# Kernel optimization log

Hardware: AMD Instinct MI355X
Metric: run time of the kernel (lower is better)

The kernel has to match this reference:

```python
import jax, jax.numpy as jnp
import numpy as np

H = 16      # num_heads
D = 1024    # input_dim
F = 4096    # feed_forward_hidden_size
B, S = 8, 4096
EPS = 1e-6


def _ln(x, g, b):
    mu = jnp.mean(x, axis=-1, keepdims=True)
    var = jnp.mean(jnp.square(x - mu), axis=-1, keepdims=True)
    return (x - mu) * jax.lax.rsqrt(var + EPS) * g + b


def _attn(Q, K, V):
    # per-head attention; original scales by sqrt(input_dim), NOT sqrt(head_dim)
    b, sq, d = Q.shape
    sk = K.shape[1]
    dh = d // H
    Qh = Q.reshape(b, sq, H, dh)
    Kh = K.reshape(b, sk, H, dh)
    Vh = V.reshape(b, sk, H, dh)
    scores = jnp.einsum('bqhd,bkhd->bhqk', Qh, Kh) / jnp.sqrt(jnp.float32(d))
    w = jax.nn.softmax(scores, axis=-1)
    return jnp.einsum('bhqk,bkhd->bqhd', w, Vh).reshape(b, sq, d)


def setup_inputs() -> dict:
    key = jax.random.key(0)
    ks = jax.random.split(key, 10)
    sc = 0.02
    np.random.seed(42)
    decode_input = jnp.asarray(np.random.random([B, 1, D]).astype(np.float32))
    return {
        'key': jax.random.normal(ks[0], (B, S, D), jnp.float32),
        'value': jax.random.normal(ks[1], (B, S, D), jnp.float32),
        'decode_input': decode_input,
        'Wq': jax.random.normal(ks[2], (D, D), jnp.float32) * sc,
        'bq': jnp.zeros((D,), jnp.float32),
        'Wk': jax.random.normal(ks[3], (D, D), jnp.float32) * sc,
        'bk': jnp.zeros((D,), jnp.float32),
        'Wv': jax.random.normal(ks[4], (D, D), jnp.float32) * sc,
        'bv': jnp.zeros((D,), jnp.float32),
        'Wo': jax.random.normal(ks[5], (D, D), jnp.float32) * sc,
        'bo': jnp.zeros((D,), jnp.float32),
        'W1': jax.random.normal(ks[6], (D, F), jnp.float32) * sc,
        'b1': jnp.zeros((F,), jnp.float32),
        'W2': jax.random.normal(ks[7], (F, D), jnp.float32) * sc,
        'b2': jnp.zeros((D,), jnp.float32),
        'ln2_g': jnp.ones((D,), jnp.float32),
        'ln2_b': jnp.zeros((D,), jnp.float32),
        'lnf_g': jnp.ones((D,), jnp.float32),
        'lnf_b': jnp.zeros((D,), jnp.float32),
    }


def reference(key, value, decode_input, Wq, bq, Wk, bk, Wv, bv, Wo, bo,
              W1, b1, W2, b2, ln2_g, ln2_b, lnf_g, lnf_b):
    # K/V projections shared by both attention calls (original reuses mha_1)
    K = key @ Wk + bk            # [B,S,D]
    V = value @ Wv + bv          # [B,S,D]

    # mha_1: self-attention of decode_input would use its own K/V, but here
    # q=k=v=decode_input for the first call
    Q1 = decode_input @ Wq + bq
    K1 = decode_input @ Wk + bk
    V1 = decode_input @ Wv + bv
    mha1_out = _attn(Q1, K1, V1) @ Wo + bo   # [B,1,D]
    # note: layer_norm_mha_1 output is computed in original but never used

    # second call (original buggily calls mha_1 again): q=mha1_out (un-normed)
    Q2 = mha1_out @ Wq + bq
    mha2_out = _attn(Q2, K, V) @ Wo + bo     # [B,1,D]
    x = _ln(mha2_out + decode_input, ln2_g, ln2_b)

    ff = jax.nn.relu(x @ W1 + b1) @ W2 + b2
    return _ln(ff + x, lnf_g, lnf_b)
```

## Files before the change

### kernel.cpp

```cpp
#include <hip/hip_runtime.h>
#include <hip/hip_bf16.h>

#define NB 8
#define NS 4096
#define ND 1024
#define NH 16
#define NF 4096

typedef __attribute__((ext_vector_type(8))) short s16x8;
typedef __attribute__((ext_vector_type(4))) float f32x4;

__device__ __forceinline__ short f2bfs(float x) {
    __hip_bfloat16 h = __float2bfloat16(x);
    return *reinterpret_cast<short*>(&h);
}

__device__ __forceinline__ s16x8 pack8(float4 a, float4 b) {
    s16x8 r;
    r[0]=f2bfs(a.x); r[1]=f2bfs(a.y); r[2]=f2bfs(a.z); r[3]=f2bfs(a.w);
    r[4]=f2bfs(b.x); r[5]=f2bfs(b.y); r[6]=f2bfs(b.z); r[7]=f2bfs(b.w);
    return r;
}


template<int KC>
__global__ void __launch_bounds__(256) mvV_k(const float* __restrict__ x,
        const float* __restrict__ W, int K, int Cout, float* __restrict__ Pout)
{
    __shared__ float xs[KC * 8];
    int tid = threadIdx.x;
    int c = blockIdx.x * 256 + tid;
    int k0 = blockIdx.y * KC;
    for (int i = tid; i < KC * 8; i += 256) {
        int k = i >> 3, b = i & 7;
        xs[i] = x[(size_t)b * K + k0 + k];
    }
    __syncthreads();
    const float* Wp = W + (size_t)k0 * Cout + c;
    float acc[8] = {0,0,0,0,0,0,0,0};
    #pragma unroll 16
    for (int k = 0; k < KC; ++k) {
        float wv = Wp[(size_t)k * Cout];
        float4 x0 = *(const float4*)&xs[k * 8];
        float4 x1 = *(const float4*)&xs[k * 8 + 4];
        acc[0] += x0.x * wv; acc[1] += x0.y * wv; acc[2] += x0.z * wv; acc[3] += x0.w * wv;
        acc[4] += x1.x * wv; acc[5] += x1.y * wv; acc[6] += x1.z * wv; acc[7] += x1.w * wv;
    }
    float* op = Pout + ((size_t)blockIdx.y * 8) * Cout + c;
    #pragma unroll
    for (int b = 0; b < 8; ++b) op[(size_t)b * Cout] = acc[b];
}

template<int KC, int NP, int RELU>
__global__ void __launch_bounds__(256) mvP_k(const float* __restrict__ P,
        const float* __restrict__ bias, const float* __restrict__ W,
        int K, int Cout, float* __restrict__ Pout)
{
    __shared__ float xs[KC * 8];
    int tid = threadIdx.x;
    int c = blockIdx.x * 256 + tid;
    int k0 = blockIdx.y * KC;
    for (int i = tid; i < KC * 8; i += 256) {
        int b = i / KC, k = i % KC;
        float t = bias[k0 + k];
        #pragma unroll 8
        for (int p = 0; p < NP; ++p) t += P[((size_t)(p * 8 + b)) * K + k0 + k];
        if (RELU) t = fmaxf(t, 0.f);
        xs[k * 8 + b] = t;
    }
    __syncthreads();
    const float* Wp = W + (size_t)k0 * Cout + c;
    float acc[8] = {0,0,0,0,0,0,0,0};
    #pragma unroll 16
    for (int k = 0; k < KC; ++k) {
        float wv = Wp[(size_t)k * Cout];
        float4 x0 = *(const float4*)&xs[k * 8];
        float4 x1 = *(const float4*)&xs[k * 8 + 4];
        acc[0] += x0.x * wv; acc[1] += x0.y * wv; acc[2] += x0.z * wv; acc[3] += x0.w * wv;
        acc[4] += x1.x * wv; acc[5] += x1.y * wv; acc[6] += x1.z * wv; acc[7] += x1.w * wv;
    }
    float* op = Pout + ((size_t)blockIdx.y * 8) * Cout + c;
    #pragma unroll
    for (int b = 0; b < 8; ++b) op[(size_t)b * Cout] = acc[b];
}

__global__ void __launch_bounds__(256) u_k(const float* __restrict__ P,
        const float* __restrict__ bq, const float* __restrict__ Wk,
        unsigned short* __restrict__ u16)
{
    int bh = blockIdx.x;
    int b = bh >> 4, h = bh & 15;
    int lane = threadIdx.x & 63, wv = threadIdx.x >> 6;
    int cc = h * 64 + lane;
    float q = bq[cc];
    #pragma unroll 8
    for (int p = 0; p < 64; ++p) q += P[((size_t)(p * 8 + b)) * 1024 + cc];
    int dbase = blockIdx.y * 256;
    #pragma unroll 4
    for (int d = dbase + wv; d < dbase + 256; d += 4) {
        float v = Wk[(size_t)d * 1024 + cc] * q;
        for (int off = 32; off; off >>= 1) v += __shfl_down(v, off);
        if (lane == 0) u16[(size_t)bh * 1024 + d] = (unsigned short)f2bfs(v);
    }
}

__global__ void __launch_bounds__(256) lnp_k(const float* __restrict__ P, int np,
        const float* __restrict__ bias, const float* __restrict__ add,
        const float* __restrict__ g, const float* __restrict__ be,
        float* __restrict__ out)
{
    int b = blockIdx.x, tid = threadIdx.x;
    __shared__ float sd[4];
    int c = tid * 4;
    f32x4 t = *(const f32x4*)&bias[c];
    t += *(const f32x4*)&add[(size_t)b * 1024 + c];
    #pragma unroll 8
    for (int p = 0; p < np; ++p)
        t += *(const f32x4*)&P[((size_t)(p * 8 + b)) * 1024 + c];
    float loc = t[0] + t[1] + t[2] + t[3];
    for (int off = 32; off; off >>= 1) loc += __shfl_down(loc, off);
    if ((tid & 63) == 0) sd[tid >> 6] = loc;
    __syncthreads();
    float mu = (sd[0] + sd[1] + sd[2] + sd[3]) * (1.f / 1024.f);
    __syncthreads();
    f32x4 d = t - mu;
    float v = d[0]*d[0] + d[1]*d[1] + d[2]*d[2] + d[3]*d[3];
    for (int off = 32; off; off >>= 1) v += __shfl_down(v, off);
    if ((tid & 63) == 0) sd[tid >> 6] = v;
    __syncthreads();
    float var = (sd[0] + sd[1] + sd[2] + sd[3]) * (1.f / 1024.f);
    float rs = rsqrtf(var + 1e-6f);
    f32x4 gg = *(const f32x4*)&g[c];
    f32x4 bb = *(const f32x4*)&be[c];
    f32x4 o = d * rs * gg + bb;
    *(f32x4*)&out[(size_t)b * 1024 + c] = o;
}

__global__ void __launch_bounds__(256) attn_k(const float* __restrict__ key,
        const float* __restrict__ value, const unsigned short* __restrict__ u16,
        float* __restrict__ plp, float* __restrict__ dnm)
{
    __shared__ __align__(16) unsigned short ul[16][1032];
    __shared__ float pl[16][64];
    int b = blockIdx.x, ch = blockIdx.y, tid = threadIdx.x;
    int s0 = ch * 64;

    const uint4* src = (const uint4*)(u16 + (size_t)b * NH * 1024);
    for (int v = tid; v < 2048; v += 256) {
        int h = v >> 7, col = (v & 127) * 8;
        *(uint4*)&ul[h][col] = src[v];
    }
    __syncthreads();

    {
        int lane = tid & 63, wv = tid >> 6;
        int r = lane & 15, g = lane >> 4;
        const float* kp0 = key + ((size_t)(b * NS + s0 + wv * 16 + r)) * ND + g * 8;
        f32x4 acc = {0.f, 0.f, 0.f, 0.f};
        float4 c0, c1, c2, c3, n0, n1, n2, n3;
        c0 = *(const float4*)(kp0);      c1 = *(const float4*)(kp0 + 4);
        c2 = *(const float4*)(kp0 + 32); c3 = *(const float4*)(kp0 + 36);
        #pragma unroll
        for (int k = 0; k < 1024; k += 64) {
            if (k + 64 < 1024) {
                const float* p = kp0 + k + 64;
                n0 = *(const float4*)(p);      n1 = *(const float4*)(p + 4);
                n2 = *(const float4*)(p + 32); n3 = *(const float4*)(p + 36);
            }
            s16x8 a0 = *(const s16x8*)&ul[r][k + g * 8];
            acc = __builtin_amdgcn_mfma_f32_16x16x32_bf16(a0, pack8(c0, c1), acc, 0, 0, 0);
            s16x8 a1 = *(const s16x8*)&ul[r][k + 32 + g * 8];
            acc = __builtin_amdgcn_mfma_f32_16x16x32_bf16(a1, pack8(c2, c3), acc, 0, 0, 0);
            c0 = n0; c1 = n1; c2 = n2; c3 = n3;
        }
        const float scl = 1.f / 32.f;
        #pragma unroll
        for (int j = 0; j < 4; ++j) {
            int h = g * 4 + j;
            pl[h][wv * 16 + r] = __expf(acc[j] * scl);
        }
    }
    __syncthreads();

    if (tid < 16) {
        float s = 0.f;
        #pragma unroll 16
        for (int si = 0; si < 64; ++si) s += pl[tid][si];
        dnm[((size_t)(ch * 8 + b)) * 16 + tid] = s;
    }

    {
        const float* vp = value + ((size_t)(b * NS + s0)) * ND + tid * 4;
        f32x4 acc[16];
        #pragma unroll
        for (int h = 0; h < 16; ++h) acc[h] = (f32x4){0.f, 0.f, 0.f, 0.f};
        f32x4 v0,v1,v2,v3,v4,v5,v6,v7;
        v0 = *(const f32x4*)(vp + 0*ND); v1 = *(const f32x4*)(vp + 1*ND);
        v2 = *(const f32x4*)(vp + 2*ND); v3 = *(const f32x4*)(vp + 3*ND);
        v4 = *(const f32x4*)(vp + 4*ND); v5 = *(const f32x4*)(vp + 5*ND);
        v6 = *(const f32x4*)(vp + 6*ND); v7 = *(const f32x4*)(vp + 7*ND);
        for (int g = 0; g < 64; g += 8) {
            f32x4 n0,n1,n2,n3,n4,n5,n6,n7;
            if (g + 8 < 64) {
                const float* p = vp + (size_t)(g + 8) * ND;
                n0 = *(const f32x4*)(p + 0*ND); n1 = *(const f32x4*)(p + 1*ND);
                n2 = *(const f32x4*)(p + 2*ND); n3 = *(const f32x4*)(p + 3*ND);
                n4 = *(const f32x4*)(p + 4*ND); n5 = *(const f32x4*)(p + 5*ND);
                n6 = *(const f32x4*)(p + 6*ND); n7 = *(const f32x4*)(p + 7*ND);
            }
            #pragma unroll
            for (int h = 0; h < 16; ++h) {
                f32x4 wa = *(const f32x4*)&pl[h][g];
                f32x4 wb = *(const f32x4*)&pl[h][g + 4];
                acc[h] += v0 * wa[0] + v1 * wa[1] + v2 * wa[2] + v3 * wa[3]
                        + v4 * wb[0] + v5 * wb[1] + v6 * wb[2] + v7 * wb[3];
            }
            v0 = n0; v1 = n1; v2 = n2; v3 = n3;
            v4 = n4; v5 = n5; v6 = n6; v7 = n7;
        }
        float* o = plp + ((size_t)((ch * 8 + b) * 16)) * 1024 + tid * 4;
        #pragma unroll
        for (int h = 0; h < 16; ++h) *(f32x4*)(o + (size_t)h * 1024) = acc[h];
    }
}

template<int KC, int NCH>
__global__ void __launch_bounds__(256) mvH_k(const float* __restrict__ plp,
        const float* __restrict__ dnm, const float* __restrict__ W,
        float* __restrict__ Pout)
{
    __shared__ float xs[4 * KC * 8];
    int tid = threadIdx.x, lane = tid & 63, wv = tid >> 6;
    int c = blockIdx.x * 256 + tid;
    int k0 = blockIdx.y * KC;
    int h = blockIdx.x * 4 + wv;
    float den = 0.f;
    if (lane < 8) {
        #pragma unroll 8
        for (int ch = 0; ch < NCH; ++ch)
            den += dnm[((size_t)(ch * 8 + lane)) * 16 + h];
    }
    float inv8 = (lane < 8) ? 1.f / den : 0.f;
    for (int i = lane; i < 8 * KC; i += 64) {
        int b = i / KC, k = i % KC;
        float t = 0.f;
        #pragma unroll 8
        for (int ch = 0; ch < NCH; ++ch)
            t += plp[((size_t)((ch * 8 + b) * 16 + h)) * 1024 + k0 + k];
        xs[wv * 8 * KC + k * 8 + b] = t * __shfl(inv8, b);
    }
    __syncthreads();
    const float* Wp = W + (size_t)k0 * 1024 + c;
    float acc[8] = {0,0,0,0,0,0,0,0};
    #pragma unroll 16
    for (int k = 0; k < KC; ++k) {
        float wvv = Wp[(size_t)k * 1024];
        float4 x0 = *(const float4*)&xs[wv * 8 * KC + k * 8];
        float4 x1 = *(const float4*)&xs[wv * 8 * KC + k * 8 + 4];
        acc[0] += x0.x * wvv; acc[1] += x0.y * wvv; acc[2] += x0.z * wvv; acc[3] += x0.w * wvv;
        acc[4] += x1.x * wvv; acc[5] += x1.y * wvv; acc[6] += x1.z * wvv; acc[7] += x1.w * wvv;
    }
    float* op = Pout + ((size_t)blockIdx.y * 8) * 1024 + c;
    #pragma unroll
    for (int b = 0; b < 8; ++b) op[(size_t)b * 1024] = acc[b];
}

extern "C" void kernel_launch(void* const* d_in, const int* in_sizes, int n_in,
                              void* d_out, int out_size, void* d_ws, size_t ws_size,
                              hipStream_t stream)
{
    const float* key   = (const float*)d_in[0];
    const float* value = (const float*)d_in[1];
    const float* dec   = (const float*)d_in[2];
    const float* Wq = (const float*)d_in[3];  const float* bq = (const float*)d_in[4];
    const float* Wk = (const float*)d_in[5];
    const float* Wv = (const float*)d_in[7];  const float* bv = (const float*)d_in[8];
    const float* Wo = (const float*)d_in[9];  const float* bo = (const float*)d_in[10];
    const float* W1 = (const float*)d_in[11]; const float* b1 = (const float*)d_in[12];
    const float* W2 = (const float*)d_in[13]; const float* b2 = (const float*)d_in[14];
    const float* g2 = (const float*)d_in[15]; const float* be2 = (const float*)d_in[16];
    const float* gf = (const float*)d_in[17]; const float* bef = (const float*)d_in[18];

    float* ws = (float*)d_ws;
    float* Pa   = ws;
    float* Pb   = Pa   + 524288;
    float* Pq   = Pb   + 524288;
    float* plp  = Pq   + 524288;
    float* dnm  = plp  + 8388608;
    float* Pd   = dnm  + 8192;
    float* Pe   = Pd   + 524288;
    float* Pff1 = Pe   + 524288;
    float* Pff2 = Pff1 + 524288;
    float* xbuf = Pff2 + 524288;
    unsigned short* u16 = (unsigned short*)(xbuf + 8192);
    float* outp = (float*)d_out;

    dim3 blk(256);

    mvV_k<16><<<dim3(4,64), blk, 0, stream>>>(dec, Wv, 1024, 1024, Pa);
    mvP_k<16,64,0><<<dim3(4,64), blk, 0, stream>>>(Pa, bv, Wo, 1024, 1024, Pb);
    mvP_k<16,64,0><<<dim3(4,64), blk, 0, stream>>>(Pb, bo, Wq, 1024, 1024, Pq);
    u_k<<<dim3(128,4), blk, 0, stream>>>(Pq, bq, Wk, u16);

    attn_k<<<dim3(8,64), blk, 0, stream>>>(key, value, u16, plp, dnm);

    mvH_k<16,64><<<dim3(4,64), blk, 0, stream>>>(plp, dnm, Wv, Pd);
    mvP_k<16,64,0><<<dim3(4,64), blk, 0, stream>>>(Pd, bv, Wo, 1024, 1024, Pe);
    lnp_k<<<dim3(8), blk, 0, stream>>>(Pe, 64, bo, dec, g2, be2, xbuf);

    mvV_k<64><<<dim3(16,16), blk, 0, stream>>>(xbuf, W1, 1024, 4096, Pff1);
    mvP_k<64,16,1><<<dim3(4,64), blk, 0, stream>>>(Pff1, b1, W2, 4096, 1024, Pff2);
    lnp_k<<<dim3(8), blk, 0, stream>>>(Pff2, 64, b2, xbuf, gf, bef, outp);

    (void)in_sizes; (void)n_in; (void)out_size; (void)ws_size;
}
```

Measured before the change: 178.7 us.

## Split fused attention into separate scores and value-pooling kernels with wider grid

The single attention kernel, which computed key scores and value pooling in one block, is split into two kernels. The scores kernel deepens its key prefetch to 128 columns and writes the exponentiated scores to a global buffer. The pooling kernel splits the value dimension in halves and each 64-row chunk across two thread groups that are reduced in shared memory, giving twice as many blocks and a higher occupancy hint. This aims to expose more parallelism and memory-level concurrency for streaming the 268MB of key/value, at the cost of an extra launch and a small global round-trip for the weights.

Measured after the change: 179.0 us. About the same (+0.1%).

```diff
diff --git a/kernel.cpp b/kernel.cpp
--- a/kernel.cpp
+++ b/kernel.cpp
@@ -136,91 +136,110 @@
     *(f32x4*)&out[(size_t)b * 1024 + c] = o;
 }
 
-__global__ void __launch_bounds__(256) attn_k(const float* __restrict__ key,
-        const float* __restrict__ value, const unsigned short* __restrict__ u16,
-        float* __restrict__ plp, float* __restrict__ dnm)
+__global__ void __launch_bounds__(256) scoresx_k(const float* __restrict__ key,
+        const unsigned short* __restrict__ u16, float* __restrict__ wexp,
+        float* __restrict__ dnm)
 {
     __shared__ __align__(16) unsigned short ul[16][1032];
-    __shared__ float pl[16][64];
+    __shared__ float pls[16][64];
     int b = blockIdx.x, ch = blockIdx.y, tid = threadIdx.x;
     int s0 = ch * 64;
-
     const uint4* src = (const uint4*)(u16 + (size_t)b * NH * 1024);
     for (int v = tid; v < 2048; v += 256) {
         int h = v >> 7, col = (v & 127) * 8;
         *(uint4*)&ul[h][col] = src[v];
     }
     __syncthreads();
-
-    {
-        int lane = tid & 63, wv = tid >> 6;
-        int r = lane & 15, g = lane >> 4;
-        const float* kp0 = key + ((size_t)(b * NS + s0 + wv * 16 + r)) * ND + g * 8;
-        f32x4 acc = {0.f, 0.f, 0.f, 0.f};
-        float4 c0, c1, c2, c3, n0, n1, n2, n3;
-        c0 = *(const float4*)(kp0);      c1 = *(const float4*)(kp0 + 4);
-        c2 = *(const float4*)(kp0 + 32); c3 = *(const float4*)(kp0 + 36);
-        #pragma unroll
-        for (int k = 0; k < 1024; k += 64) {
-            if (k + 64 < 1024) {
-                const float* p = kp0 + k + 64;
-                n0 = *(const float4*)(p);      n1 = *(const float4*)(p + 4);
-                n2 = *(const float4*)(p + 32); n3 = *(const float4*)(p + 36);
-            }
-            s16x8 a0 = *(const s16x8*)&ul[r][k + g * 8];
-            acc = __builtin_amdgcn_mfma_f32_16x16x32_bf16(a0, pack8(c0, c1), acc, 0, 0, 0);
-            s16x8 a1 = *(const s16x8*)&ul[r][k + 32 + g * 8];
-            acc = __builtin_amdgcn_mfma_f32_16x16x32_bf16(a1, pack8(c2, c3), acc, 0, 0, 0);
-            c0 = n0; c1 = n1; c2 = n2; c3 = n3;
+    int lane = tid & 63, wv = tid >> 6;
+    int r = lane & 15, g = lane >> 4;
+    const float* kp0 = key + ((size_t)(b * NS + s0 + wv * 16 + r)) * ND + g * 8;
+    f32x4 acc = {0.f, 0.f, 0.f, 0.f};
+    float4 c0,c1,c2,c3,c4,c5,c6,c7, n0,n1,n2,n3,n4,n5,n6,n7;
+    c0 = *(const float4*)(kp0);       c1 = *(const float4*)(kp0 + 4);
+    c2 = *(const float4*)(kp0 + 32);  c3 = *(const float4*)(kp0 + 36);
+    c4 = *(const float4*)(kp0 + 64);  c5 = *(const float4*)(kp0 + 68);
+    c6 = *(const float4*)(kp0 + 96);  c7 = *(const float4*)(kp0 + 100);
+    #pragma unroll
+    for (int k = 0; k < 1024; k += 128) {
+        if (k + 128 < 1024) {
+            const float* p = kp0 + k + 128;
+            n0 = *(const float4*)(p);       n1 = *(const float4*)(p + 4);
+            n2 = *(const float4*)(p + 32);  n3 = *(const float4*)(p + 36);
+            n4 = *(const float4*)(p + 64);  n5 = *(const float4*)(p + 68);
+            n6 = *(const float4*)(p + 96);  n7 = *(const float4*)(p + 100);
         }
-        const float scl = 1.f / 32.f;
-        #pragma unroll
-        for (int j = 0; j < 4; ++j) {
-            int h = g * 4 + j;
-            pl[h][wv * 16 + r] = __expf(acc[j] * scl);
-        }
-    }
-    __syncthreads();
-
+        s16x8 a0 = *(const s16x8*)&ul[r][k + g * 8];
+        acc = __builtin_amdgcn_mfma_f32_16x16x32_bf16(a0, pack8(c0, c1), acc, 0, 0, 0);
+        s16x8 a1 = *(const s16x8*)&ul[r][k + 32 + g * 8];
+        acc = __builtin_amdgcn_mfma_f32_16x16x32_bf16(a1, pack8(c2, c3), acc, 0, 0, 0);
+        s16x8 a2 = *(const s16x8*)&ul[r][k + 64 + g * 8];
+        acc = __builtin_amdgcn_mfma_f32_16x16x32_bf16(a2, pack8(c4, c5), acc, 0, 0, 0);
+        s16x8 a3 = *(const s16x8*)&ul[r][k + 96 + g * 8];
+        acc = __builtin_amdgcn_mfma_f32_16x16x32_bf16(a3, pack8(c6, c7), acc, 0, 0, 0);
+        c0 = n0; c1 = n1; c2 = n2; c3 = n3;
+        c4 = n4; c5 = n5; c6 = n6; c7 = n7;
+    }
+    const float scl = 1.f / 32.f;
+    #pragma unroll
+    for (int j = 0; j < 4; ++j) {
+        int h = g * 4 + j;
+        float e = __expf(acc[j] * scl);
+        wexp[((size_t)(b * NH + h)) * NS + s0 + wv * 16 + r] = e;
+        pls[h][wv * 16 + r] = e;
+    }
+    __syncthreads();
     if (tid < 16) {
         float s = 0.f;
         #pragma unroll 16
-        for (int si = 0; si < 64; ++si) s += pl[tid][si];
+        for (int si = 0; si < 64; ++si) s += pls[tid][si];
         dnm[((size_t)(ch * 8 + b)) * 16 + tid] = s;
     }
-
+}
+
+__global__ void __launch_bounds__(256, 4) poolx_k(const float* __restrict__ value,
+        const float* __restrict__ wexp, float* __restrict__ plp)
+{
+    __shared__ float pl[16][64];
+    __shared__ f32x4 red[16][128];
+    int b = blockIdx.x, ch = blockIdx.y, dh = blockIdx.z, tid = threadIdx.x;
+    int s0 = ch * 64;
     {
-        const float* vp = value + ((size_t)(b * NS + s0)) * ND + tid * 4;
-        f32x4 acc[16];
+        int h = tid >> 4, col = (tid & 15) * 4;
+        *(f32x4*)&pl[h][col] = *(const f32x4*)&wexp[((size_t)(b * NH + h)) * NS + s0 + col];
+    }
+    __syncthreads();
+    int dt = tid & 127, sg = tid >> 7;
+    const float* vp = value + ((size_t)(b * NS + s0 + sg * 32)) * ND + dh * 512 + dt * 4;
+    f32x4 acc[16];
+    #pragma unroll
+    for (int h = 0; h < 16; ++h) acc[h] = (f32x4){0.f, 0.f, 0.f, 0.f};
+    f32x4 v0, v1, v2, v3;
+    v0 = *(const f32x4*)(vp + 0*ND); v1 = *(const f32x4*)(vp + 1*ND);
+    v2 = *(const f32x4*)(vp + 2*ND); v3 = *(const f32x4*)(vp + 3*ND);
+    for (int g = 0; g < 32; g += 4) {
+        f32x4 n0, n1, n2, n3;
+        if (g + 4 < 32) {
+            const float* p = vp + (size_t)(g + 4) * ND;
+            n0 = *(const f32x4*)(p + 0*ND); n1 = *(const f32x4*)(p + 1*ND);
+            n2 = *(const f32x4*)(p + 2*ND); n3 = *(const f32x4*)(p + 3*ND);
+        }
         #pragma unroll
-        for (int h = 0; h < 16; ++h) acc[h] = (f32x4){0.f, 0.f, 0.f, 0.f};
-        f32x4 v0,v1,v2,v3,v4,v5,v6,v7;
-        v0 = *(const f32x4*)(vp + 0*ND); v1 = *(const f32x4*)(vp + 1*ND);
-        v2 = *(const f32x4*)(vp + 2*ND); v3 = *(const f32x4*)(vp + 3*ND);
-        v4 = *(const f32x4*)(vp + 4*ND); v5 = *(const f32x4*)(vp + 5*ND);
-        v6 = *(const f32x4*)(vp + 6*ND); v7 = *(const f32x4*)(vp + 7*ND);
-        for (int g = 0; g < 64; g += 8) {
-            f32x4 n0,n1,n2,n3,n4,n5,n6,n7;
-            if (g + 8 < 64) {
-                const float* p = vp + (size_t)(g + 8) * ND;
-                n0 = *(const f32x4*)(p + 0*ND); n1 = *(const f32x4*)(p + 1*ND);
-                n2 = *(const f32x4*)(p + 2*ND); n3 = *(const f32x4*)(p + 3*ND);
-                n4 = *(const f32x4*)(p + 4*ND); n5 = *(const f32x4*)(p + 5*ND);
-                n6 = *(const f32x4*)(p + 6*ND); n7 = *(const f32x4*)(p + 7*ND);
-            }
-            #pragma unroll
-            for (int h = 0; h < 16; ++h) {
-                f32x4 wa = *(const f32x4*)&pl[h][g];
-                f32x4 wb = *(const f32x4*)&pl[h][g + 4];
-                acc[h] += v0 * wa[0] + v1 * wa[1] + v2 * wa[2] + v3 * wa[3]
-                        + v4 * wb[0] + v5 * wb[1] + v6 * wb[2] + v7 * wb[3];
-            }
-            v0 = n0; v1 = n1; v2 = n2; v3 = n3;
-            v4 = n4; v5 = n5; v6 = n6; v7 = n7;
+        for (int h = 0; h < 16; ++h) {
+            f32x4 wa = *(const f32x4*)&pl[h][sg * 32 + g];
+            acc[h] += v0 * wa[0] + v1 * wa[1] + v2 * wa[2] + v3 * wa[3];
         }
-        float* o = plp + ((size_t)((ch * 8 + b) * 16)) * 1024 + tid * 4;
+        v0 = n0; v1 = n1; v2 = n2; v3 = n3;
+    }
+    if (sg == 1) {
         #pragma unroll
-        for (int h = 0; h < 16; ++h) *(f32x4*)(o + (size_t)h * 1024) = acc[h];
+        for (int h = 0; h < 16; ++h) red[h][dt] = acc[h];
+    }
+    __syncthreads();
+    if (sg == 0) {
+        float* o = plp + ((size_t)((ch * 8 + b) * 16)) * 1024 + dh * 512 + dt * 4;
+        #pragma unroll
+        for (int h = 0; h < 16; ++h)
+            *(f32x4*)(o + (size_t)h * 1024) = acc[h] + red[h][dt];
     }
 }
 
@@ -285,7 +304,8 @@
     float* Pa   = ws;
     float* Pb   = Pa   + 524288;
     float* Pq   = Pb   + 524288;
-    float* plp  = Pq   + 524288;
+    float* wexp = Pq   + 524288;
+    float* plp  = wexp + 524288;
     float* dnm  = plp  + 8388608;
     float* Pd   = dnm  + 8192;
     float* Pe   = Pd   + 524288;
@@ -302,7 +322,8 @@
     mvP_k<16,64,0><<<dim3(4,64), blk, 0, stream>>>(Pb, bo, Wq, 1024, 1024, Pq);
     u_k<<<dim3(128,4), blk, 0, stream>>>(Pq, bq, Wk, u16);
 
-    attn_k<<<dim3(8,64), blk, 0, stream>>>(key, value, u16, plp, dnm);
+    scoresx_k<<<dim3(8,64), blk, 0, stream>>>(key, u16, wexp, dnm);
+    poolx_k<<<dim3(8,64,2), blk, 0, stream>>>(value, wexp, plp);
 
     mvH_k<16,64><<<dim3(4,64), blk, 0, stream>>>(plp, dnm, Wv, Pd);
     mvP_k<16,64,0><<<dim3(4,64), blk, 0, stream>>>(Pd, bv, Wo, 1024, 1024, Pe);
```
